# Performance work log

Hardware: AMD Instinct MI355X
Metric: run time of the kernel (lower is better)

Reference implementation:

```python
import jax, jax.numpy as jnp
import numpy as np

LAMB = 1.0
EPS = 1e-16


def setup_inputs() -> dict:
    key = jax.random.key(0)
    kx, km = jax.random.split(key)
    N, D, K = 262144, 128, 64
    x = jax.random.normal(kx, (N, D), dtype=jnp.float32)
    m = jax.random.normal(km, (K, D), dtype=jnp.float32)
    m = m / jnp.linalg.norm(m, axis=1, keepdims=True)  # unit-norm rows like __init__
    return {"x": x, "m": m}


def _entropy(p):
    # replicate torch.where clamping
    p = jnp.where(p <= 0, EPS, p)
    p = jnp.where(p >= 1, 1.0 - EPS, p)
    return -jnp.sum(p * jnp.log(p), axis=-1)


def _p(x, m):
    d2 = (jnp.sum(x * x, axis=-1, keepdims=True)
          - 2.0 * x @ m.T
          + jnp.sum(m * m, axis=-1))  # [N, K]
    return jax.nn.softmax(-d2, axis=-1)


def reference(x, m):
    p = _p(x, m)                      # [N, K]
    intra = jnp.mean(_entropy(p))     # scalar
    mu = jnp.mean(m, axis=0)          # [D]
    p_inter = _p(mu[None, :], m)[0]   # [K]
    inter = _entropy(p_inter)
    total = intra - LAMB * inter
    return (total, intra, inter)
```

## Files before the change

kernel.cpp:

```cpp
#include <hip/hip_runtime.h>

#define D 128
#define K 64

typedef __attribute__((ext_vector_type(8))) short short8;
typedef __attribute__((ext_vector_type(4))) float f32x4;

__device__ inline short f2bf(float f) {
  union { float f; unsigned u; } v; v.f = f;
  unsigned u = v.u;
  return (short)((u + 0x7fffu + ((u >> 16) & 1u)) >> 16);
}

template<int CTRL>
__device__ inline float dpp_ror(float x) {
  return __builtin_bit_cast(float, __builtin_amdgcn_update_dpp(
      0, __builtin_bit_cast(int, x), CTRL, 0xF, 0xF, true));
}
__device__ inline float rowsum16(float v) {
  v += dpp_ror<0x121>(v);
  v += dpp_ror<0x122>(v);
  v += dpp_ror<0x124>(v);
  v += dpp_ror<0x128>(v);
  return v;
}
__device__ inline float rowmax16(float v) {
  v = fmaxf(v, dpp_ror<0x121>(v));
  v = fmaxf(v, dpp_ror<0x122>(v));
  v = fmaxf(v, dpp_ror<0x124>(v));
  v = fmaxf(v, dpp_ror<0x128>(v));
  return v;
}

__global__ void prep_kernel(const float* __restrict__ m, float* ws) {
  int tid = threadIdx.x;
  if (tid < 16) ws[tid] = 0.0f;
  if (tid < K) {
    const float* mr = m + tid * D;
    float s = 0.f;
    for (int d = 0; d < D; ++d) s += mr[d] * mr[d];
    ws[16 + tid] = s;
  }
  short* mb = (short*)(ws + 128);
  for (int i = tid; i < K * D; i += blockDim.x) mb[i] = f2bf(2.0f * m[i]);
}

__launch_bounds__(256, 4)
__global__ void main_kernel(const float* __restrict__ x, float* ws, int nTiles, int totalWaves) {
  __shared__ short8 bsm[1024];
  const float* mnorm = ws + 16;
  const short8* mbv = (const short8*)(ws + 128);
  for (int i = threadIdx.x; i < 1024; i += blockDim.x)
    bsm[i ^ ((i >> 4) & 7)] = mbv[i];
  __syncthreads();

  const int lane = threadIdx.x & 63;
  const int lid  = lane & 15;
  const int quad = lane >> 4;

  float mn[4];
#pragma unroll
  for (int jt = 0; jt < 4; ++jt) mn[jt] = mnorm[jt * 16 + lid];

  int cbase[4];
#pragma unroll
  for (int kk = 0; kk < 4; ++kk)
    cbase[kk] = (lid * 16 + kk * 4 + quad) ^ (lid & 7);

  const int wave = blockIdx.x * (blockDim.x >> 6) + (threadIdx.x >> 6);
  const size_t laneOff = (size_t)lid * D + quad * 8;
  float hacc = 0.f;

  f32x4 ld[8];
  {
    const float* xb = x + (size_t)wave * (16 * D) + laneOff;
#pragma unroll
    for (int kk = 0; kk < 4; ++kk) {
      ld[2 * kk]     = *(const f32x4*)(xb + kk * 32);
      ld[2 * kk + 1] = *(const f32x4*)(xb + kk * 32 + 4);
    }
  }

  for (int t = wave; t < nTiles; t += totalWaves) {
    short8 a[4];
#pragma unroll
    for (int kk = 0; kk < 4; ++kk) {
      f32x4 v0 = ld[2 * kk], v1 = ld[2 * kk + 1];
      short8 av;
      av[0] = f2bf(v0[0]); av[1] = f2bf(v0[1]); av[2] = f2bf(v0[2]); av[3] = f2bf(v0[3]);
      av[4] = f2bf(v1[0]); av[5] = f2bf(v1[1]); av[6] = f2bf(v1[2]); av[7] = f2bf(v1[3]);
      a[kk] = av;
    }

    int tn = t + totalWaves;
    if (tn < nTiles) {
      const float* xb = x + (size_t)tn * (16 * D) + laneOff;
#pragma unroll
      for (int kk = 0; kk < 4; ++kk) {
        ld[2 * kk]     = *(const f32x4*)(xb + kk * 32);
        ld[2 * kk + 1] = *(const f32x4*)(xb + kk * 32 + 4);
      }
    }

    f32x4 acc[4];
#pragma unroll
    for (int jt = 0; jt < 4; ++jt) acc[jt] = (f32x4){0.f, 0.f, 0.f, 0.f};
#pragma unroll
    for (int kk = 0; kk < 4; ++kk)
#pragma unroll
      for (int jt = 0; jt < 4; ++jt) {
        short8 b = bsm[cbase[kk] + jt * 256];
        acc[jt] = __builtin_amdgcn_mfma_f32_16x16x32_bf16(a[kk], b, acc[jt], 0, 0, 0);
      }

#pragma unroll
    for (int r = 0; r < 4; ++r) {
      float s0 = acc[0][r] - mn[0];
      float s1 = acc[1][r] - mn[1];
      float s2 = acc[2][r] - mn[2];
      float s3 = acc[3][r] - mn[3];
      float mx = rowmax16(fmaxf(fmaxf(s0, s1), fmaxf(s2, s3)));
      float t0 = s0 - mx, t1 = s1 - mx, t2 = s2 - mx, t3 = s3 - mx;
      float e0 = __expf(t0), e1 = __expf(t1), e2 = __expf(t2), e3 = __expf(t3);
      float S0 = rowsum16((e0 + e1) + (e2 + e3));
      float S1 = rowsum16((t0 * e0 + t1 * e1) + (t2 * e2 + t3 * e3));
      float H = __logf(S0) - S1 / S0;
      if (lid == 0) hacc += H;
    }
  }

  for (int off = 1; off < 64; off <<= 1) hacc += __shfl_xor(hacc, off, 64);
  __shared__ float red[4];
  if (lane == 0) red[threadIdx.x >> 6] = hacc;
  __syncthreads();
  if (threadIdx.x == 0) atomicAdd(ws, red[0] + red[1] + red[2] + red[3]);
}

__global__ void final_kernel(const float* __restrict__ m, const float* ws, float* out, int nRows) {
  __shared__ float mu[D];
  int lane = threadIdx.x;
  for (int d = lane; d < D; d += 64) {
    float s = 0.f;
    for (int j = 0; j < K; ++j) s += m[j * D + d];
    mu[d] = s * (1.0f / K);
  }
  __syncthreads();
  const float* mr = m + lane * D;
  float dot = 0.f;
  for (int d = 0; d < D; ++d) dot += mu[d] * mr[d];
  float s = 2.f * dot - ws[16 + lane];
  float mx = s;
  for (int off = 1; off < 64; off <<= 1) mx = fmaxf(mx, __shfl_xor(mx, off, 64));
  float t = s - mx;
  float e = __expf(t);
  float S0 = e, S1 = t * e;
  for (int off = 1; off < 64; off <<= 1) {
    S0 += __shfl_xor(S0, off, 64);
    S1 += __shfl_xor(S1, off, 64);
  }
  float inter = __logf(S0) - S1 / S0;
  if (lane == 0) {
    float intra = ws[0] / (float)nRows;
    out[0] = intra - inter;
    out[1] = intra;
    out[2] = inter;
  }
}

extern "C" void kernel_launch(void* const* d_in, const int* in_sizes, int n_in,
                              void* d_out, int out_size, void* d_ws, size_t ws_size,
                              hipStream_t stream) {
  const float* x = (const float*)d_in[0];
  const float* m = (const float*)d_in[1];
  float* ws = (float*)d_ws;
  float* out = (float*)d_out;
  const int N = in_sizes[0] / D;
  const int nTiles = N / 16;

  prep_kernel<<<1, 256, 0, stream>>>(m, ws);

  const int blocks = 1024;
  const int totalWaves = blocks * 4;
  main_kernel<<<blocks, 256, 0, stream>>>(x, ws, nTiles, totalWaves);

  final_kernel<<<1, 64, 0, stream>>>(m, ws, out, N);
}
```

Baseline: 226.2 us.

## Coalesce x loads and stage bf16 A-tiles through swizzled LDS

Global loads of x now have each wave read contiguous 1KB rows per instruction (lane*4 floats) instead of the scattered per-row MFMA fragment pattern. Each wave converts the values to bf16, writes them to a per-wave XOR-swizzled LDS buffer, and reads them back in MFMA operand layout. This targets memory coalescing on a bandwidth-bound stream, at the cost of an extra LDS write and read per tile. There is no explicit barrier between the LDS write and read, so correctness relies on intra-wave ordering.

```diff
diff --git a/kernel.cpp b/kernel.cpp
--- a/kernel.cpp
+++ b/kernel.cpp
@@ -4,6 +4,7 @@
 #define K 64
 
 typedef __attribute__((ext_vector_type(8))) short short8;
+typedef __attribute__((ext_vector_type(4))) short bf4;
 typedef __attribute__((ext_vector_type(4))) float f32x4;
 
 __device__ inline short f2bf(float f) {
@@ -48,6 +49,8 @@
 __launch_bounds__(256, 4)
 __global__ void main_kernel(const float* __restrict__ x, float* ws, int nTiles, int totalWaves) {
   __shared__ short8 bsm[1024];
+  __shared__ char asmem[4][4096];
+
   const float* mnorm = ws + 16;
   const short8* mbv = (const short8*)(ws + 128);
   for (int i = threadIdx.x; i < 1024; i += blockDim.x)
@@ -57,6 +60,8 @@
   const int lane = threadIdx.x & 63;
   const int lid  = lane & 15;
   const int quad = lane >> 4;
+  const int wid  = threadIdx.x >> 6;
+  char* amem = asmem[wid];
 
   float mn[4];
 #pragma unroll
@@ -67,40 +72,46 @@
   for (int kk = 0; kk < 4; ++kk)
     cbase[kk] = (lid * 16 + kk * 4 + quad) ^ (lid & 7);
 
-  const int wave = blockIdx.x * (blockDim.x >> 6) + (threadIdx.x >> 6);
-  const size_t laneOff = (size_t)lid * D + quad * 8;
+  const int hi = lane >> 5;
+  const int wc = (lane & 31) >> 1;
+  const int wh = lane & 1;
+
+  int ra[4];
+#pragma unroll
+  for (int kk = 0; kk < 4; ++kk)
+    ra[kk] = lid * 256 + ((((kk << 2) | quad) ^ lid) << 4);
+
+  const int wave = blockIdx.x * (blockDim.x >> 6) + wid;
   float hacc = 0.f;
 
   f32x4 ld[8];
   {
-    const float* xb = x + (size_t)wave * (16 * D) + laneOff;
+    const float* xb = x + (size_t)wave * (16 * D) + lane * 4;
 #pragma unroll
-    for (int kk = 0; kk < 4; ++kk) {
-      ld[2 * kk]     = *(const f32x4*)(xb + kk * 32);
-      ld[2 * kk + 1] = *(const f32x4*)(xb + kk * 32 + 4);
-    }
+    for (int p = 0; p < 8; ++p) ld[p] = *(const f32x4*)(xb + p * 256);
   }
 
   for (int t = wave; t < nTiles; t += totalWaves) {
-    short8 a[4];
 #pragma unroll
-    for (int kk = 0; kk < 4; ++kk) {
-      f32x4 v0 = ld[2 * kk], v1 = ld[2 * kk + 1];
-      short8 av;
-      av[0] = f2bf(v0[0]); av[1] = f2bf(v0[1]); av[2] = f2bf(v0[2]); av[3] = f2bf(v0[3]);
-      av[4] = f2bf(v1[0]); av[5] = f2bf(v1[1]); av[6] = f2bf(v1[2]); av[7] = f2bf(v1[3]);
-      a[kk] = av;
+    for (int p = 0; p < 8; ++p) {
+      f32x4 v = ld[p];
+      bf4 s;
+      s[0] = f2bf(v[0]); s[1] = f2bf(v[1]); s[2] = f2bf(v[2]); s[3] = f2bf(v[3]);
+      int r = 2 * p + hi;
+      *(bf4*)(amem + r * 256 + ((wc ^ r) << 4) + wh * 8) = s;
     }
 
     int tn = t + totalWaves;
     if (tn < nTiles) {
-      const float* xb = x + (size_t)tn * (16 * D) + laneOff;
+      const float* xb = x + (size_t)tn * (16 * D) + lane * 4;
 #pragma unroll
-      for (int kk = 0; kk < 4; ++kk) {
-        ld[2 * kk]     = *(const f32x4*)(xb + kk * 32);
-        ld[2 * kk + 1] = *(const f32x4*)(xb + kk * 32 + 4);
-      }
+      for (int p = 0; p < 8; ++p) ld[p] = *(const f32x4*)(xb + p * 256);
     }
+
+    short8 a[4];
+#pragma unroll
+    for (int kk = 0; kk < 4; ++kk)
+      a[kk] = *(const short8*)(amem + ra[kk]);
 
     f32x4 acc[4];
 #pragma unroll
@@ -131,7 +142,7 @@
 
   for (int off = 1; off < 64; off <<= 1) hacc += __shfl_xor(hacc, off, 64);
   __shared__ float red[4];
-  if (lane == 0) red[threadIdx.x >> 6] = hacc;
+  if (lane == 0) red[wid] = hacc;
   __syncthreads();
   if (threadIdx.x == 0) atomicAdd(ws, red[0] + red[1] + red[2] + red[3]);
 }
```

Result: faster. 215.2 us (-4.9%).
